# Kernel tuning notes

Measured on AMD Instinct MI355X. Metric: run time of the kernel, lower is better.

## Reference

```python
import jax, jax.numpy as jnp
import numpy as np

FIN, FOUT, FH, LAT = 64, 64, 128, 512
B, H, Wd = 16, 128, 128
SIZES = [FH * FIN, FH * FH, FH * FH, FOUT * FH, FOUT * FIN, FH, FH, FH, FOUT, FOUT]
KTOT = sum(SIZES)


def setup_inputs() -> dict:
    key = jax.random.key(0)
    k1, k2, k3, k4 = jax.random.split(key, 4)
    x = jax.random.normal(k1, (B, FIN, H, Wd), dtype=jnp.float32)
    lat = jax.random.normal(k2, (B, LAT), dtype=jnp.float32)
    W = jax.random.normal(k3, (KTOT, LAT), dtype=jnp.float32) * 0.02
    b = jax.random.normal(k4, (KTOT,), dtype=jnp.float32) * 0.02
    return {"x": x, "lat": lat, "W": W, "b": b}


def _split_kernels(ks):
    # ks: [B, KTOT] hypernetwork output -> per-sample 1x1 conv weights + biases
    offs = np.cumsum([0] + SIZES)
    parts = [ks[:, offs[i]:offs[i + 1]] for i in range(10)]
    k_in = parts[0].reshape(B, FH, FIN) / jnp.sqrt(FH)
    k_mida = parts[1].reshape(B, FH, FH) / jnp.sqrt(FH)
    k_midb = parts[2].reshape(B, FH, FH) / jnp.sqrt(FH)
    k_out = parts[3].reshape(B, FOUT, FH) / jnp.sqrt(FOUT)
    k_short = parts[4].reshape(B, FOUT, FIN) / jnp.sqrt(FOUT)
    b_in = parts[5].reshape(B, FH, 1, 1)
    b_mida = parts[6].reshape(B, FH, 1, 1)
    b_midb = parts[7].reshape(B, FH, 1, 1)
    b_out = parts[8].reshape(B, FOUT, 1, 1)
    b_short = parts[9].reshape(B, FOUT, 1, 1)
    return k_in, k_mida, k_midb, k_out, k_short, b_in, b_mida, b_midb, b_out, b_short


def _pconv(k, xv):
    # per-sample 1x1 conv: k [B,O,I], xv [B,I,H,W] -> [B,O,H,W]
    return jnp.einsum('boi,bihw->bohw', k, xv)


def reference(x, lat, W, b):
    ks = lat @ W.T + b  # [B, KTOT]
    k_in, k_mida, k_midb, k_out, k_short, b_in, b_mida, b_midb, b_out, b_short = _split_kernels(ks)
    x_s = _pconv(k_short, x) + b_short
    h = jax.nn.relu(_pconv(k_in, x) + b_in)
    h = jax.nn.relu(_pconv(k_mida, h) + b_mida)
    h = jax.nn.relu(_pconv(k_midb, h) + b_midb)
    out = _pconv(k_out, h) + b_out + x_s
    return out
```

## Files before the change

kernel.cpp:

```cpp
#include <hip/hip_runtime.h>
#include <cstdint>
#include <cstddef>


typedef short bf16x8 __attribute__((ext_vector_type(8)));
typedef float f32x16 __attribute__((ext_vector_type(16)));

#define DEVFN static __device__ __forceinline__

constexpr int WELEM      = 53248;
constexpr int NSAMP      = 16;
constexpr size_t WS_WSHORTS = (size_t)WELEM;
constexpr size_t WS_WBYTES_TOT = (size_t)NSAMP * WELEM * 2;

DEVFN unsigned bf16rne(float f) {
  unsigned u = __builtin_bit_cast(unsigned, f);
  return (u + 0x7fffu + ((u >> 16) & 1u)) >> 16;
}
DEVFN unsigned pk2(float lo, float hi) {
  return bf16rne(lo) | (bf16rne(hi) << 16);
}

__global__ __launch_bounds__(128) void hyper_gemm(
    const float* __restrict__ lat, const float* __restrict__ W,
    const float* __restrict__ bias, unsigned short* __restrict__ w_ws,
    float* __restrict__ b_ws) {
  __shared__ float Wl[64 * 68];
  const int t = threadIdx.x;
  const int n0 = blockIdx.x * 64;
  const int c = t & 63;
  const int half = __builtin_amdgcn_readfirstlane(t >> 6);

  const float* wp = W + (size_t)n0 * 512;
  float4 ld[8];

  auto loadW = [&](int kc) {
#pragma unroll
    for (int i = 0; i < 8; ++i) {
      const int u = t + 128 * i;
      const int row = u >> 4, c4 = u & 15;
      ld[i] = *(const float4*)(wp + (size_t)row * 512 + kc * 64 + c4 * 4);
    }
  };

  float acc[16];
#pragma unroll
  for (int b = 0; b < 16; ++b) acc[b] = 0.f;

  loadW(0);
#pragma unroll 1
  for (int kc = 0; kc < 8; ++kc) {
#pragma unroll
    for (int i = 0; i < 8; ++i) {
      const int u = t + 128 * i;
      const int row = u >> 4, c4 = u & 15;
      *(float4*)&Wl[row * 68 + c4 * 4] = ld[i];
    }
    __syncthreads();
    if (kc < 7) loadW(kc + 1);

    const int kb = kc * 64 + half * 32;
#pragma unroll
    for (int j4 = 0; j4 < 8; ++j4) {
      const float4 wv = *(const float4*)&Wl[c * 68 + half * 32 + j4 * 4];
      const float* lp = lat + kb + j4 * 4;
#pragma unroll
      for (int b = 0; b < 16; ++b) {
        const float4 lv = *(const float4*)(lp + (size_t)b * 512);
        acc[b] = fmaf(wv.x, lv.x, acc[b]);
        acc[b] = fmaf(wv.y, lv.y, acc[b]);
        acc[b] = fmaf(wv.z, lv.z, acc[b]);
        acc[b] = fmaf(wv.w, lv.w, acc[b]);
      }
    }
    __syncthreads();
  }

  float* red = Wl;
  if (half == 1) {
#pragma unroll
    for (int b = 0; b < 16; ++b) red[c * 17 + b] = acc[b];
  }
  __syncthreads();
  if (t < 64) {
#pragma unroll
    for (int b = 0; b < 16; ++b) acc[b] += red[c * 17 + b];

    const int n = n0 + c;
    const float bv = bias[n];
    if (n >= 53248) {
      const int j = n - 53248;
#pragma unroll
      for (int b = 0; b < 16; ++b) b_ws[b * 512 + j] = acc[b] + bv;
      return;
    }
    int fragbase, off, kbits;
    float scale;
    if (n < 8192)       { fragbase = 0;  off = 0;     kbits = 6; scale = 0.08838834764831845f; }
    else if (n < 24576) { fragbase = 16; off = 8192;  kbits = 7; scale = 0.08838834764831845f; }
    else if (n < 40960) { fragbase = 48; off = 24576; kbits = 7; scale = 0.08838834764831845f; }
    else if (n < 49152) { fragbase = 80; off = 40960; kbits = 7; scale = 0.125f; }
    else                { fragbase = 96; off = 49152; kbits = 6; scale = 0.125f; }
    const int r = n - off;
    const int m = r >> kbits;
    const int k = r & ((1 << kbits) - 1);
    const int mt = m >> 5, ks = k >> 4;
    const int lane = (m & 31) + 32 * ((k >> 3) & 1);
    const int j = k & 7;
    const int frag = fragbase + mt * (1 << (kbits - 4)) + ks;
    const size_t eoff = (size_t)frag * 512 + lane * 8 + j;
#pragma unroll
    for (int b = 0; b < 16; ++b) {
      const float v = (acc[b] + bv) * scale;
      w_ws[(size_t)b * WS_WSHORTS + eoff] = (unsigned short)bf16rne(v);
    }
  }
}


DEVFN f32x16 bias_init(const float* bl, int mt, int lh) {
  f32x16 a;
#pragma unroll
  for (int g = 0; g < 4; ++g) {
    const float4 bv = *(const float4*)&bl[mt * 32 + 8 * g + 4 * lh];
    a[4 * g + 0] = bv.x; a[4 * g + 1] = bv.y;
    a[4 * g + 2] = bv.z; a[4 * g + 3] = bv.w;
  }
  return a;
}

DEVFN void write_h(short* hb, int mt, int l31, int lh, const f32x16& a0,
                   const f32x16& a1) {
#pragma unroll
  for (int g = 0; g < 4; ++g) {
    const int kstep = mt * 2 + (g >> 1);
    const int sub = g & 1;
    const int base = (kstep * 2) * 512 + (l31 + 32 * sub) * 8 + lh * 4;
    uint2 w0, w1;
    w0.x = pk2(fmaxf(a0[4 * g + 0], 0.f), fmaxf(a0[4 * g + 1], 0.f));
    w0.y = pk2(fmaxf(a0[4 * g + 2], 0.f), fmaxf(a0[4 * g + 3], 0.f));
    w1.x = pk2(fmaxf(a1[4 * g + 0], 0.f), fmaxf(a1[4 * g + 1], 0.f));
    w1.y = pk2(fmaxf(a1[4 * g + 2], 0.f), fmaxf(a1[4 * g + 3], 0.f));
    *(uint2*)&hb[base] = w0;
    *(uint2*)&hb[base + 512] = w1;
  }
}

#define MFMA32(A, B, C) __builtin_amdgcn_mfma_f32_32x32x16_bf16((A), (B), (C), 0, 0, 0)

__global__ __launch_bounds__(256, 1) void dyn_conv(
    const float* __restrict__ x, const unsigned short* __restrict__ w_ws,
    const float* __restrict__ b_ws, float* __restrict__ out) {
  __shared__ short wl[72 * 512];
  __shared__ float bl[512];
  __shared__ short hl[4][8192];

  const int s = blockIdx.x >> 4;
  const int chunk = blockIdx.x & 15;
  const int tid = threadIdx.x;
  const int wv = tid >> 6;
  const int l = tid & 63;
  const int l31 = l & 31;
  const int lh = l >> 5;

  const unsigned short* wbase = w_ws + (size_t)s * WS_WSHORTS;

  for (int f = wv; f < 72; f += 4) {
    const int fg = (f < 16) ? f : f + 32;
    *(int4*)&wl[f * 512 + l * 8] = *(const int4*)&wbase[fg * 512 + l * 8];
  }
  bl[tid] = b_ws[s * 512 + tid];
  bl[tid + 256] = b_ws[s * 512 + tid + 256];

  bf16x8 Am[32];
#pragma unroll
  for (int i = 0; i < 32; ++i)
    Am[i] = *(const bf16x8*)&wbase[(16 + i) * 512 + l * 8];

  const float* xbase = x + (size_t)(s * 64) * 16384;
  float xr[2][4][8];
  auto load_xr = [&](int it) {
    const int px0 = chunk * 1024 + it * 256 + wv * 64;
#pragma unroll
    for (int nt = 0; nt < 2; ++nt) {
#pragma unroll
      for (int ks = 0; ks < 4; ++ks) {
        const float* xp =
            xbase + (size_t)(ks * 16 + lh * 8) * 16384 + px0 + nt * 32 + l31;
#pragma unroll
        for (int j = 0; j < 8; ++j) xr[nt][ks][j] = xp[(size_t)j * 16384];
      }
    }
  };
  load_xr(0);

  __syncthreads();

  short* hb = &hl[wv][0];

#pragma unroll 1
  for (int it = 0; it < 4; ++it) {
    const int px0 = chunk * 1024 + it * 256 + wv * 64;

    bf16x8 xf[2][4];
#pragma unroll
    for (int nt = 0; nt < 2; ++nt) {
#pragma unroll
      for (int ks = 0; ks < 4; ++ks) {
        union { unsigned u[4]; bf16x8 v8; } uu;
#pragma unroll
        for (int j = 0; j < 4; ++j)
          uu.u[j] = pk2(xr[nt][ks][2 * j], xr[nt][ks][2 * j + 1]);
        xf[nt][ks] = uu.v8;
      }
    }
    if (it < 3) load_xr(it + 1);

#pragma unroll
    for (int mt = 0; mt < 4; ++mt) {
      f32x16 a0 = bias_init(bl + 0, mt, lh);
      f32x16 a1 = a0;
#pragma unroll
      for (int ks = 0; ks < 4; ++ks) {
        const bf16x8 A = *(const bf16x8*)&wl[(mt * 4 + ks) * 512 + l * 8];
        a0 = MFMA32(A, xf[0][ks], a0);
        a1 = MFMA32(A, xf[1][ks], a1);
      }
      write_h(hb, mt, l31, lh, a0, a1);
    }

    bf16x8 hB[16];

#pragma unroll
    for (int i = 0; i < 16; ++i) hB[i] = *(const bf16x8*)&hb[i * 512 + l * 8];
#pragma unroll
    for (int mt = 0; mt < 4; ++mt) {
      f32x16 a0 = bias_init(bl + 128, mt, lh);
      f32x16 a1 = a0;
#pragma unroll
      for (int ks = 0; ks < 8; ++ks) {
        a0 = MFMA32(Am[mt * 8 + ks], hB[ks * 2 + 0], a0);
        a1 = MFMA32(Am[mt * 8 + ks], hB[ks * 2 + 1], a1);
      }
      write_h(hb, mt, l31, lh, a0, a1);
    }

#pragma unroll
    for (int i = 0; i < 16; ++i) hB[i] = *(const bf16x8*)&hb[i * 512 + l * 8];
#pragma unroll
    for (int mt = 0; mt < 4; ++mt) {
      f32x16 a0 = bias_init(bl + 256, mt, lh);
      f32x16 a1 = a0;
#pragma unroll
      for (int ks = 0; ks < 8; ++ks) {
        const bf16x8 A = *(const bf16x8*)&wl[(16 + mt * 8 + ks) * 512 + l * 8];
        a0 = MFMA32(A, hB[ks * 2 + 0], a0);
        a1 = MFMA32(A, hB[ks * 2 + 1], a1);
      }
      write_h(hb, mt, l31, lh, a0, a1);
    }

#pragma unroll
    for (int i = 0; i < 16; ++i) hB[i] = *(const bf16x8*)&hb[i * 512 + l * 8];
#pragma unroll
    for (int mt = 0; mt < 2; ++mt) {
      f32x16 a0 = bias_init(bl + 384, mt, lh);
      {
        const f32x16 bs = bias_init(bl + 448, mt, lh);
#pragma unroll
        for (int e = 0; e < 16; ++e) a0[e] += bs[e];
      }
      f32x16 a1 = a0;
#pragma unroll
      for (int ks = 0; ks < 4; ++ks) {
        const bf16x8 A = *(const bf16x8*)&wl[(64 + mt * 4 + ks) * 512 + l * 8];
        a0 = MFMA32(A, xf[0][ks], a0);
        a1 = MFMA32(A, xf[1][ks], a1);
      }
#pragma unroll
      for (int ks = 0; ks < 8; ++ks) {
        const bf16x8 A = *(const bf16x8*)&wl[(48 + mt * 8 + ks) * 512 + l * 8];
        a0 = MFMA32(A, hB[ks * 2 + 0], a0);
        a1 = MFMA32(A, hB[ks * 2 + 1], a1);
      }
#pragma unroll
      for (int g = 0; g < 4; ++g) {
#pragma unroll
        for (int q = 0; q < 4; ++q) {
          const int row = mt * 32 + 8 * g + 4 * lh + q;
          float* op = out + (size_t)(s * 64 + row) * 16384 + px0 + l31;
          op[0]  = a0[4 * g + q];
          op[32] = a1[4 * g + q];
        }
      }
    }
  }
}

extern "C" void kernel_launch(void* const* d_in, const int* in_sizes, int n_in,
                              void* d_out, int out_size, void* d_ws,
                              size_t ws_size, hipStream_t stream) {
  (void)in_sizes; (void)n_in; (void)out_size; (void)ws_size;
  const float* x   = (const float*)d_in[0];
  const float* lat = (const float*)d_in[1];
  const float* W   = (const float*)d_in[2];
  const float* b   = (const float*)d_in[3];
  unsigned short* w_ws = (unsigned short*)d_ws;
  float* b_ws = (float*)((char*)d_ws + WS_WBYTES_TOT);
  float* out = (float*)d_out;

  hyper_gemm<<<dim3(840), dim3(128), 0, stream>>>(lat, W, b, w_ws, b_ws);
  dyn_conv<<<dim3(256), dim3(256), 0, stream>>>(x, w_ws, b_ws, out);
}
```

Measured before the change: 320.9 us.

## Compute hypernetwork GEMM with split-bf16 MFMA instead of scalar FP32 FMA

Replaces the scalar FP32 hypernetwork GEMM with MFMA 16x16x32 bf16 instructions. Each wave handles 16 output rows, and three MFMAs (hi*hi, hi*lo, lo*hi) keep near-FP32 accuracy. A small new lat_prep kernel pre-splits the latent matrix into hi/lo bf16 fragments in the workspace. W is still read once as fp32 and split in registers, so the goal is to cut ALU time in a GEMM dominated by W bandwidth, at the cost of an extra launch and some precision loss from dropping the lo*lo term.

```diff
diff --git a/kernel.cpp b/kernel.cpp
--- a/kernel.cpp
+++ b/kernel.cpp
@@ -4,14 +4,17 @@
 
 
 typedef short bf16x8 __attribute__((ext_vector_type(8)));
+typedef float f32x4  __attribute__((ext_vector_type(4)));
 typedef float f32x16 __attribute__((ext_vector_type(16)));
 
 #define DEVFN static __device__ __forceinline__
 
 constexpr int WELEM      = 53248;
-constexpr int NSAMP      = 16;
 constexpr size_t WS_WSHORTS = (size_t)WELEM;
-constexpr size_t WS_WBYTES_TOT = (size_t)NSAMP * WELEM * 2;
+constexpr size_t WS_WBYTES_TOT = (size_t)16 * WELEM * 2;
+constexpr size_t WS_BOFF  = WS_WBYTES_TOT;
+constexpr size_t WS_AHOFF = WS_BOFF + 16 * 512 * 4;
+constexpr size_t WS_ALOFF = WS_AHOFF + 16384;
 
 DEVFN unsigned bf16rne(float f) {
   unsigned u = __builtin_bit_cast(unsigned, f);
@@ -21,99 +24,113 @@
   return bf16rne(lo) | (bf16rne(hi) << 16);
 }
 
-__global__ __launch_bounds__(128) void hyper_gemm(
-    const float* __restrict__ lat, const float* __restrict__ W,
-    const float* __restrict__ bias, unsigned short* __restrict__ w_ws,
-    float* __restrict__ b_ws) {
-  __shared__ float Wl[64 * 68];
-  const int t = threadIdx.x;
-  const int n0 = blockIdx.x * 64;
-  const int c = t & 63;
-  const int half = __builtin_amdgcn_readfirstlane(t >> 6);
-
-  const float* wp = W + (size_t)n0 * 512;
-  float4 ld[8];
-
-  auto loadW = [&](int kc) {
-#pragma unroll
-    for (int i = 0; i < 8; ++i) {
-      const int u = t + 128 * i;
-      const int row = u >> 4, c4 = u & 15;
-      ld[i] = *(const float4*)(wp + (size_t)row * 512 + kc * 64 + c4 * 4);
-    }
-  };
-
-  float acc[16];
-#pragma unroll
-  for (int b = 0; b < 16; ++b) acc[b] = 0.f;
-
-  loadW(0);
-#pragma unroll 1
-  for (int kc = 0; kc < 8; ++kc) {
-#pragma unroll
-    for (int i = 0; i < 8; ++i) {
-      const int u = t + 128 * i;
-      const int row = u >> 4, c4 = u & 15;
-      *(float4*)&Wl[row * 68 + c4 * 4] = ld[i];
-    }
-    __syncthreads();
-    if (kc < 7) loadW(kc + 1);
-
-    const int kb = kc * 64 + half * 32;
-#pragma unroll
-    for (int j4 = 0; j4 < 8; ++j4) {
-      const float4 wv = *(const float4*)&Wl[c * 68 + half * 32 + j4 * 4];
-      const float* lp = lat + kb + j4 * 4;
-#pragma unroll
-      for (int b = 0; b < 16; ++b) {
-        const float4 lv = *(const float4*)(lp + (size_t)b * 512);
-        acc[b] = fmaf(wv.x, lv.x, acc[b]);
-        acc[b] = fmaf(wv.y, lv.y, acc[b]);
-        acc[b] = fmaf(wv.z, lv.z, acc[b]);
-        acc[b] = fmaf(wv.w, lv.w, acc[b]);
-      }
-    }
-    __syncthreads();
-  }
-
-  float* red = Wl;
-  if (half == 1) {
-#pragma unroll
-    for (int b = 0; b < 16; ++b) red[c * 17 + b] = acc[b];
-  }
-  __syncthreads();
-  if (t < 64) {
-#pragma unroll
-    for (int b = 0; b < 16; ++b) acc[b] += red[c * 17 + b];
-
-    const int n = n0 + c;
-    const float bv = bias[n];
-    if (n >= 53248) {
-      const int j = n - 53248;
-#pragma unroll
-      for (int b = 0; b < 16; ++b) b_ws[b * 512 + j] = acc[b] + bv;
-      return;
-    }
-    int fragbase, off, kbits;
-    float scale;
-    if (n < 8192)       { fragbase = 0;  off = 0;     kbits = 6; scale = 0.08838834764831845f; }
-    else if (n < 24576) { fragbase = 16; off = 8192;  kbits = 7; scale = 0.08838834764831845f; }
-    else if (n < 40960) { fragbase = 48; off = 24576; kbits = 7; scale = 0.08838834764831845f; }
-    else if (n < 49152) { fragbase = 80; off = 40960; kbits = 7; scale = 0.125f; }
-    else                { fragbase = 96; off = 49152; kbits = 6; scale = 0.125f; }
-    const int r = n - off;
-    const int m = r >> kbits;
-    const int k = r & ((1 << kbits) - 1);
-    const int mt = m >> 5, ks = k >> 4;
-    const int lane = (m & 31) + 32 * ((k >> 3) & 1);
-    const int j = k & 7;
-    const int frag = fragbase + mt * (1 << (kbits - 4)) + ks;
-    const size_t eoff = (size_t)frag * 512 + lane * 8 + j;
-#pragma unroll
-    for (int b = 0; b < 16; ++b) {
-      const float v = (acc[b] + bv) * scale;
-      w_ws[(size_t)b * WS_WSHORTS + eoff] = (unsigned short)bf16rne(v);
-    }
+__global__ __launch_bounds__(256) void lat_prep(
+    const float* __restrict__ lat, unsigned short* __restrict__ ah_ws,
+    unsigned short* __restrict__ al_ws) {
+  const int id = blockIdx.x * 256 + threadIdx.x;
+  const int s = id >> 6, l = id & 63;
+  const int m = l & 15, q = l >> 4;
+  const float* ap = lat + m * 512 + s * 32 + q * 8;
+  float f[8];
+#pragma unroll
+  for (int j = 0; j < 8; ++j) f[j] = ap[j];
+  unsigned H[4], L[4];
+#pragma unroll
+  for (int p = 0; p < 4; ++p) {
+    const unsigned u0 = __builtin_bit_cast(unsigned, f[2 * p]);
+    const unsigned u1 = __builtin_bit_cast(unsigned, f[2 * p + 1]);
+    const unsigned h0 = u0 & 0xFFFF0000u, h1 = u1 & 0xFFFF0000u;
+    H[p] = (h0 >> 16) | h1;
+    const float lo0 = f[2 * p] - __builtin_bit_cast(float, h0);
+    const float lo1 = f[2 * p + 1] - __builtin_bit_cast(float, h1);
+    L[p] = pk2(lo0, lo1);
+  }
+  *(uint4*)&ah_ws[(size_t)(s * 64 + l) * 8] = make_uint4(H[0], H[1], H[2], H[3]);
+  *(uint4*)&al_ws[(size_t)(s * 64 + l) * 8] = make_uint4(L[0], L[1], L[2], L[3]);
+}
+
+#define MFMA16(A, B, C) __builtin_amdgcn_mfma_f32_16x16x32_bf16((A), (B), (C), 0, 0, 0)
+
+__global__ __launch_bounds__(256, 2) void hyper_gemm(
+    const float* __restrict__ W, const float* __restrict__ bias,
+    const unsigned short* __restrict__ ah_ws,
+    const unsigned short* __restrict__ al_ws,
+    unsigned short* __restrict__ w_ws, float* __restrict__ b_ws) {
+  const int tid = threadIdx.x;
+  const int wv = tid >> 6;
+  const int l = tid & 63;
+  const int q = l >> 4;
+  const int g = blockIdx.x * 4 + wv;
+  const int n0 = g * 16;
+  const int n = n0 + (l & 15);
+
+  bf16x8 Ah[16], Al[16];
+#pragma unroll
+  for (int s = 0; s < 16; ++s) {
+    Ah[s] = *(const bf16x8*)&ah_ws[(size_t)(s * 64 + l) * 8];
+    Al[s] = *(const bf16x8*)&al_ws[(size_t)(s * 64 + l) * 8];
+  }
+
+  const float* bp = W + (size_t)n * 512 + q * 8;
+  float4 ld[8][2];
+#pragma unroll
+  for (int s = 0; s < 8; ++s) {
+    ld[s][0] = *(const float4*)(bp + s * 32);
+    ld[s][1] = *(const float4*)(bp + s * 32 + 4);
+  }
+
+  f32x4 acc = {0.f, 0.f, 0.f, 0.f};
+#pragma unroll
+  for (int s = 0; s < 16; ++s) {
+    const float4 b0 = ld[s & 7][0];
+    const float4 b1 = ld[s & 7][1];
+    if (s < 8) {
+      ld[s][0] = *(const float4*)(bp + (s + 8) * 32);
+      ld[s][1] = *(const float4*)(bp + (s + 8) * 32 + 4);
+    }
+    const float f[8] = {b0.x, b0.y, b0.z, b0.w, b1.x, b1.y, b1.z, b1.w};
+    union { unsigned u[4]; bf16x8 v; } BH, BL;
+#pragma unroll
+    for (int p = 0; p < 4; ++p) {
+      const unsigned u0 = __builtin_bit_cast(unsigned, f[2 * p]);
+      const unsigned u1 = __builtin_bit_cast(unsigned, f[2 * p + 1]);
+      const unsigned h0 = u0 & 0xFFFF0000u, h1 = u1 & 0xFFFF0000u;
+      BH.u[p] = (h0 >> 16) | h1;
+      const float lo0 = f[2 * p] - __builtin_bit_cast(float, h0);
+      const float lo1 = f[2 * p + 1] - __builtin_bit_cast(float, h1);
+      BL.u[p] = pk2(lo0, lo1);
+    }
+    acc = MFMA16(Ah[s], BH.v, acc);
+    acc = MFMA16(Ah[s], BL.v, acc);
+    acc = MFMA16(Al[s], BH.v, acc);
+  }
+
+  const float bv = bias[n];
+  if (n0 >= 53248) {
+    const int j = n - 53248;
+#pragma unroll
+    for (int r = 0; r < 4; ++r) b_ws[(q * 4 + r) * 512 + j] = acc[r] + bv;
+    return;
+  }
+  int fragbase, off, kbits;
+  float scale;
+  if (n < 8192)       { fragbase = 0;  off = 0;     kbits = 6; scale = 0.08838834764831845f; }
+  else if (n < 24576) { fragbase = 16; off = 8192;  kbits = 7; scale = 0.08838834764831845f; }
+  else if (n < 40960) { fragbase = 48; off = 24576; kbits = 7; scale = 0.08838834764831845f; }
+  else if (n < 49152) { fragbase = 80; off = 40960; kbits = 7; scale = 0.125f; }
+  else                { fragbase = 96; off = 49152; kbits = 6; scale = 0.125f; }
+  const int r0 = n - off;
+  const int m = r0 >> kbits;
+  const int k = r0 & ((1 << kbits) - 1);
+  const int mt = m >> 5, ks = k >> 4;
+  const int lane = (m & 31) + 32 * ((k >> 3) & 1);
+  const int j = k & 7;
+  const int frag = fragbase + mt * (1 << (kbits - 4)) + ks;
+  const size_t eoff = (size_t)frag * 512 + lane * 8 + j;
+#pragma unroll
+  for (int r = 0; r < 4; ++r) {
+    const float v = (acc[r] + bv) * scale;
+    w_ws[(size_t)(q * 4 + r) * WS_WSHORTS + eoff] = (unsigned short)bf16rne(v);
   }
 }
 
@@ -306,9 +323,12 @@
   const float* W   = (const float*)d_in[2];
   const float* b   = (const float*)d_in[3];
   unsigned short* w_ws = (unsigned short*)d_ws;
-  float* b_ws = (float*)((char*)d_ws + WS_WBYTES_TOT);
+  float* b_ws = (float*)((char*)d_ws + WS_BOFF);
+  unsigned short* ah_ws = (unsigned short*)((char*)d_ws + WS_AHOFF);
+  unsigned short* al_ws = (unsigned short*)((char*)d_ws + WS_ALOFF);
   float* out = (float*)d_out;
 
-  hyper_gemm<<<dim3(840), dim3(128), 0, stream>>>(lat, W, b, w_ws, b_ws);
+  lat_prep<<<dim3(4), dim3(256), 0, stream>>>(lat, ah_ws, al_ws);
+  hyper_gemm<<<dim3(840), dim3(256), 0, stream>>>(W, b, ah_ws, al_ws, w_ws, b_ws);
   dyn_conv<<<dim3(256), dim3(256), 0, stream>>>(x, w_ws, b_ws, out);
 }
```

After: 268.2 us. -16.4%, faster.
